# Performance work log

Measured on AMD Instinct MI355X. Metric: run time of the kernel, lower is better.

## Reference

```python
import jax, jax.numpy as jnp
import numpy as np
from jax.scipy.special import logsumexp

L = 15      # DATA_MAX_SEG_LEN
K = 64      # XCRIBE_DIM
H = 16      # SEG_DIM
TAG = 32    # TAG_DIM
DUR = 4     # DURATION_DIM
NY = 15     # len(LABELS)
N = 16384   # sequence length
S = 2048    # number of gold segments
NEG = jnp.float32(-1e30)


def setup_inputs() -> dict:
    key = jax.random.key(0)
    ks = jax.random.split(key, 24)
    sL = 1.0 / np.sqrt(H)
    sV = 1.0 / np.sqrt(2 * H + TAG + DUR)
    sW = 1.0 / np.sqrt(H)

    def U(k, shape, s):
        return jax.random.uniform(k, shape, jnp.float32, -s, s)

    return dict(
        data=jax.random.normal(ks[0], (N, K), jnp.float32),
        fwd_Wih=U(ks[1], (4 * H, K), sL), fwd_Whh=U(ks[2], (4 * H, H), sL),
        fwd_bih=U(ks[3], (4 * H,), sL), fwd_bhh=U(ks[4], (4 * H,), sL),
        bwd_Wih=U(ks[5], (4 * H, K), sL), bwd_Whh=U(ks[6], (4 * H, H), sL),
        bwd_bih=U(ks[7], (4 * H,), sL), bwd_bhh=U(ks[8], (4 * H,), sL),
        fwd_h0=jax.random.normal(ks[9], (H,), jnp.float32),
        fwd_c0=jax.random.normal(ks[10], (H,), jnp.float32),
        bwd_h0=jax.random.normal(ks[11], (H,), jnp.float32),
        bwd_c0=jax.random.normal(ks[12], (H,), jnp.float32),
        Y_enc=jax.random.normal(ks[13], (NY, TAG), jnp.float32),
        Z_enc=jax.random.normal(ks[14], (L, DUR), jnp.float32),
        V_W=U(ks[15], (H, 2 * H + TAG + DUR), sV), V_b=U(ks[16], (H,), sV),
        W_W=U(ks[17], (1, H), sW), W_b=U(ks[18], (1,), sW),
        tags=jax.random.randint(ks[19], (S,), 0, NY),
        lengths=jax.random.randint(ks[20], (S,), 1, L + 1),
    )


def _lstm(xs, Wih, Whh, bih, bhh, h0, c0):
    # xs: [L, B, K] -> hidden outputs [L, B, H]; torch gate order i,f,g,o
    B = xs.shape[1]
    b = bih + bhh

    def step(carry, x):
        h, c = carry
        g = x @ Wih.T + h @ Whh.T + b
        i, f, gg, o = jnp.split(g, 4, axis=-1)
        c = jax.nn.sigmoid(f) * c + jax.nn.sigmoid(i) * jnp.tanh(gg)
        h = jax.nn.sigmoid(o) * jnp.tanh(c)
        return (h, c), h

    init = (jnp.broadcast_to(h0, (B, H)), jnp.broadcast_to(c0, (B, H)))
    _, hs = jax.lax.scan(step, init, xs)
    return hs


def reference(data, fwd_Wih, fwd_Whh, fwd_bih, fwd_bhh, fwd_h0, fwd_c0,
              bwd_Wih, bwd_Whh, bwd_bih, bwd_bhh, bwd_h0, bwd_c0,
              Y_enc, Z_enc, V_W, V_b, W_W, W_b, tags, lengths):
    n = data.shape[0]
    pos = jnp.arange(n)[:, None]      # [N,1]
    dd = jnp.arange(L)[None, :]       # [1,L]
    idx_f = jnp.minimum(pos + dd, n - 1)   # forward window indices
    idx_b = pos - dd                       # backward window indices (may be <0)

    win_f = data[idx_f].transpose(1, 0, 2)                  # [L,N,K]
    win_b = data[jnp.maximum(idx_b, 0)].transpose(1, 0, 2)  # [L,N,K]

    # fwd[i,d] = forward_precalc[i][i+d]; bwd[e,d] = backward_precalc[e-d][e]
    fwd = _lstm(win_f, fwd_Wih, fwd_Whh, fwd_bih, fwd_bhh, fwd_h0, fwd_c0).transpose(1, 0, 2)
    bwd = _lstm(win_b, bwd_Wih, bwd_Whh, bwd_bih, bwd_bhh, bwd_h0, bwd_c0).transpose(1, 0, 2)

    # gather fwd at (start=e-d, duration index d) -> aligned with end position e
    fwd_g = fwd[jnp.maximum(idx_b, 0), dd]          # [N,L,H]
    fb = jnp.concatenate([fwd_g, bwd], axis=-1)     # [N,L,2H]

    # split V across concat blocks: [fwd,bwd | Y | Z]
    V1 = V_W[:, :2 * H]; V2 = V_W[:, 2 * H:2 * H + TAG]; V3 = V_W[:, 2 * H + TAG:]
    base = fb @ V1.T + (Z_enc @ V3.T)[None, :, :] + V_b      # [N,L,H]
    ypart = Y_enc @ V2.T                                     # [NY,H]
    pre = base[:, :, None, :] + ypart[None, None, :, :]      # [N,L,NY,H]
    scores = jnp.tanh(pre) @ W_W[0] + W_b[0]                 # [N,L,NY]

    valid = idx_b >= 0
    A = jnp.where(valid, logsumexp(scores, axis=-1), NEG)    # [N,L] lse over labels

    # semi-Markov forward DP: log_alpha[i] = lse_d(log_alpha[i-d] + A[i-1,d-1])
    def dp(hist, a):  # hist[k] = log_alpha[i-1-k]
        new = logsumexp(hist + a)
        return jnp.concatenate([new[None], hist[:-1]]), new

    hist0 = jnp.full((L,), NEG, jnp.float32).at[0].set(0.0)
    _, alphas = jax.lax.scan(dp, hist0, A)
    logZ = alphas[-1]

    # gold-segment score; original never advances `chars`, so start is always 0
    gv = lengths < L
    gscores = scores[lengths - 1, lengths - 1, tags]
    indiv = jnp.sum(jnp.where(gv, gscores, 0.0))
    return logZ - indiv
```

## Files before the change

kernel.cpp:

```cpp
#include <hip/hip_runtime.h>

#define NPOS 16384
#define NEG  (-1e30f)

#define OFF_FWDH  0
#define OFF_BWDH  1966080
#define OFF_A     3932160
#define OFF_T0    4194304
#define OFF_R     4251904
#define OFF_GSC   4255504
#define OFF_CTR   4255744

struct Params {
    const float *data, *fWih, *fWhh, *fbih, *fbhh, *bWih, *bWhh, *bbih, *bbhh;
    const float *h0f, *c0f, *h0b, *c0b, *Yenc, *Zenc, *VW, *Vb, *WW, *Wb;
    const int *tags, *lengths;
    float *ws; float *out;
};

typedef _Float16 half2_t __attribute__((ext_vector_type(2)));

__device__ __forceinline__ half2_t u2h(unsigned int v) {
    return __builtin_bit_cast(half2_t, v);
}
__device__ __forceinline__ unsigned int packh(float a, float b) {
    half2_t h = { (_Float16)a, (_Float16)b };
    return __builtin_bit_cast(unsigned int, h);
}
__device__ __forceinline__ float fdot2_(unsigned int w, unsigned int x, float acc) {
    return __builtin_amdgcn_fdot2(u2h(w), u2h(x), acc, false);
}
__device__ __forceinline__ float sigf(float x) {
    return __builtin_amdgcn_rcpf(1.0f + __expf(-x));
}
__device__ __forceinline__ float tanhf_(float x) {
    return 1.0f - 2.0f * __builtin_amdgcn_rcpf(1.0f + __expf(2.0f * x));
}
__device__ __forceinline__ float lse15(const float* tv) {
    float a0 = fmaxf(tv[0], tv[1]),  a1 = fmaxf(tv[2], tv[3]);
    float a2 = fmaxf(tv[4], tv[5]),  a3 = fmaxf(tv[6], tv[7]);
    float a4 = fmaxf(tv[8], tv[9]),  a5 = fmaxf(tv[10], tv[11]);
    float a6 = fmaxf(tv[12], tv[13]);
    float b0 = fmaxf(a0, a1), b1 = fmaxf(a2, a3), b2 = fmaxf(a4, a5), b3 = fmaxf(a6, tv[14]);
    float mx = fmaxf(fmaxf(b0, b1), fmaxf(b2, b3));
    float e[15];
    #pragma unroll
    for (int i = 0; i < 15; i++) e[i] = __expf(tv[i] - mx);
    float s0 = e[0]+e[1], s1 = e[2]+e[3], s2 = e[4]+e[5], s3 = e[6]+e[7];
    float s4 = e[8]+e[9], s5 = e[10]+e[11], s6 = e[12]+e[13];
    float t0 = s0+s1, t1 = s2+s3, t2 = s4+s5, t3 = s6+e[14];
    return mx + __logf((t0+t1) + (t2+t3));
}

__global__ __launch_bounds__(512) void kA(Params p)
{
    __shared__ unsigned int xs2[78*33];
    __shared__ float xgT[64*78];
    __shared__ unsigned int hsh[2*512];
    __shared__ unsigned int wqx[2048];
    __shared__ unsigned int wqh[512];
    __shared__ float bq[64];

    const int tid  = threadIdx.x;
    const int lane = tid & 63;
    const int wq   = __builtin_amdgcn_readfirstlane(tid >> 6);
    const int dir  = blockIdx.y;
    const int P0   = blockIdx.x << 6;
    const int dbase = P0 - (dir ? 14 : 0);

    if (blockIdx.x == 0 && dir == 0 && tid == 0)
        ((unsigned int*)(p.ws + OFF_CTR))[0] = 0;

    const float* Wih = dir ? p.bWih : p.fWih;
    const float* Whh = dir ? p.bWhh : p.fWhh;
    const float* bih = dir ? p.bbih : p.fbih;
    const float* bhh = dir ? p.bbhh : p.fbhh;
    const float* h0  = dir ? p.h0b  : p.h0f;
    const float* c0  = dir ? p.c0b  : p.c0f;

    for (int e = tid; e < 2048; e += 512) {
        int k2 = e >> 6, pi = e & 63;
        int w = pi >> 3, jj = pi & 7;
        int j = ((jj >> 1) << 4) + 2*w + (jj & 1);
        wqx[e] = packh(Wih[j*64 + 2*k2], Wih[j*64 + 2*k2 + 1]);
    }
    if (tid < 512) {
        int m2 = tid >> 6, pi = tid & 63;
        int w = pi >> 3, jj = pi & 7;
        int j = ((jj >> 1) << 4) + 2*w + (jj & 1);
        wqh[tid] = packh(Whh[j*16 + 2*m2], Whh[j*16 + 2*m2 + 1]);
    }
    if (tid < 64) {
        int w = tid >> 3, jj = tid & 7;
        int j = ((jj >> 1) << 4) + 2*w + (jj & 1);
        bq[tid] = bih[j] + bhh[j];
    }
    for (int idx = tid; idx < 78*32; idx += 512) {
        int r = idx >> 5, c = idx & 31;
        int q = dbase + r;
        q = q < 0 ? 0 : (q > NPOS-1 ? NPOS-1 : q);
        float2 x2 = *(const float2*)(p.data + (size_t)q*64 + c*2);
        xs2[r*33 + c] = packh(x2.x, x2.y);
    }
    if (tid < 512) {
        int m2 = tid >> 6;
        hsh[tid] = packh(h0[2*m2], h0[2*m2 + 1]);
    }
    __syncthreads();

    #pragma unroll
    for (int pass = 0; pass < 2; pass++) {
        int r = pass*64 + lane;
        if (r < 78) {
            float acc[8];
            #pragma unroll
            for (int jj = 0; jj < 8; jj++) acc[jj] = bq[wq*8 + jj];
            #pragma unroll 8
            for (int k2 = 0; k2 < 32; k2++) {
                unsigned int xp = xs2[r*33 + k2];
                uint4 w0 = *(const uint4*)&wqx[k2*64 + wq*8];
                uint4 w1 = *(const uint4*)&wqx[k2*64 + wq*8 + 4];
                acc[0] = fdot2_(w0.x, xp, acc[0]);
                acc[1] = fdot2_(w0.y, xp, acc[1]);
                acc[2] = fdot2_(w0.z, xp, acc[2]);
                acc[3] = fdot2_(w0.w, xp, acc[3]);
                acc[4] = fdot2_(w1.x, xp, acc[4]);
                acc[5] = fdot2_(w1.y, xp, acc[5]);
                acc[6] = fdot2_(w1.z, xp, acc[6]);
                acc[7] = fdot2_(w1.w, xp, acc[7]);
            }
            #pragma unroll
            for (int jj = 0; jj < 8; jj++) xgT[(wq*8 + jj)*78 + r] = acc[jj];
        }
    }
    float cv0 = c0[wq*2], cv1 = c0[wq*2 + 1];
    unsigned int* outH = (unsigned int*)(p.ws + (dir ? OFF_BWDH : OFF_FWDH));
    __syncthreads();

    int buf = 0;
    for (int d = 0; d < 15; d++) {
        const int row = dir ? (lane + 14 - d) : (lane + d);
        float part[8];
        #pragma unroll
        for (int jj = 0; jj < 8; jj++) part[jj] = xgT[(wq*8 + jj)*78 + row];
        #pragma unroll
        for (int m2 = 0; m2 < 8; m2++) {
            unsigned int hp = hsh[buf*512 + m2*64 + lane];
            uint4 w0 = *(const uint4*)&wqh[m2*64 + wq*8];
            uint4 w1 = *(const uint4*)&wqh[m2*64 + wq*8 + 4];
            part[0] = fdot2_(w0.x, hp, part[0]);
            part[1] = fdot2_(w0.y, hp, part[1]);
            part[2] = fdot2_(w0.z, hp, part[2]);
            part[3] = fdot2_(w0.w, hp, part[3]);
            part[4] = fdot2_(w1.x, hp, part[4]);
            part[5] = fdot2_(w1.y, hp, part[5]);
            part[6] = fdot2_(w1.z, hp, part[6]);
            part[7] = fdot2_(w1.w, hp, part[7]);
        }
        float cn0 = sigf(part[2])*cv0 + sigf(part[0])*tanhf_(part[4]);
        float cn1 = sigf(part[3])*cv1 + sigf(part[1])*tanhf_(part[5]);
        cv0 = cn0; cv1 = cn1;
        float h0v = sigf(part[6])*tanhf_(cn0);
        float h1v = sigf(part[7])*tanhf_(cn1);
        unsigned int pk = packh(h0v, h1v);
        hsh[(buf^1)*512 + wq*64 + lane] = pk;
        outH[((size_t)d*NPOS + P0 + lane)*8 + wq] = pk;
        __syncthreads();
        buf ^= 1;
    }
}

__global__ __launch_bounds__(1024) void kBC(Params p)
{
    __shared__ float As[64*17];
    __shared__ unsigned int VWh[256];
    __shared__ float zbl[240];
    __shared__ float EY[240];
    const int tid = threadIdx.x;
    const int P0  = blockIdx.x << 6;
    float* ws = p.ws;

    if (tid < 240) {
        int y = tid >> 4, h = tid & 15;
        float acc = 0.f;
        for (int t = 0; t < 32; t++) acc += p.Yenc[y*32 + t] * p.VW[h*68 + 32 + t];
        EY[tid] = __expf(acc + acc);
        float z = p.Vb[h];
        for (int u = 0; u < 4; u++) z += p.Zenc[y*4 + u] * p.VW[h*68 + 64 + u];
        zbl[tid] = z;
    }
    if (tid < 256) {
        int h = tid >> 4, j2 = tid & 15;
        int col = (j2 < 8) ? 2*j2 : 16 + 2*(j2 - 8);
        VWh[tid] = packh(p.VW[h*68 + col], p.VW[h*68 + col + 1]);
    }
    __syncthreads();

    const int pl = tid & 63;
    const int d  = tid >> 6;
    const int pp = P0 + pl;
    float Aval = NEG;
    if (d < 15 && pp >= d) {
        const uint4* fptr = (const uint4*)((const unsigned int*)(ws + OFF_FWDH)
                            + ((size_t)d*NPOS + (pp - d))*8);
        const uint4* bptr = (const uint4*)((const unsigned int*)(ws + OFF_BWDH)
                            + ((size_t)d*NPOS + pp)*8);
        uint4 f0 = fptr[0], f1 = fptr[1];
        uint4 b0 = bptr[0], b1 = bptr[1];
        unsigned int fp_[8] = {f0.x, f0.y, f0.z, f0.w, f1.x, f1.y, f1.z, f1.w};
        unsigned int bp_[8] = {b0.x, b0.y, b0.z, b0.w, b1.x, b1.y, b1.z, b1.w};
        float E[16], w2[16], wsum = 0.f;
        #pragma unroll
        for (int h = 0; h < 16; h++) {
            float acc = zbl[d*16 + h];
            uint4 va = *(const uint4*)&VWh[h*16];
            uint4 vb = *(const uint4*)&VWh[h*16 + 4];
            uint4 vc = *(const uint4*)&VWh[h*16 + 8];
            uint4 vd = *(const uint4*)&VWh[h*16 + 12];
            acc = fdot2_(va.x, fp_[0], acc); acc = fdot2_(va.y, fp_[1], acc);
            acc = fdot2_(va.z, fp_[2], acc); acc = fdot2_(va.w, fp_[3], acc);
            acc = fdot2_(vb.x, fp_[4], acc); acc = fdot2_(vb.y, fp_[5], acc);
            acc = fdot2_(vb.z, fp_[6], acc); acc = fdot2_(vb.w, fp_[7], acc);
            acc = fdot2_(vc.x, bp_[0], acc); acc = fdot2_(vc.y, bp_[1], acc);
            acc = fdot2_(vc.z, bp_[2], acc); acc = fdot2_(vc.w, bp_[3], acc);
            acc = fdot2_(vd.x, bp_[4], acc); acc = fdot2_(vd.y, bp_[5], acc);
            acc = fdot2_(vd.z, bp_[6], acc); acc = fdot2_(vd.w, bp_[7], acc);
            E[h] = __expf(acc + acc);
            float w = p.WW[h];
            w2[h] = -2.0f * w;
            wsum += w;
        }
        const float cst = p.Wb[0] + wsum;
        float sc[15];
        #pragma unroll
        for (int y = 0; y < 15; y++) {
            float a = 0.f;
            #pragma unroll
            for (int h = 0; h < 16; h++)
                a = fmaf(w2[h], __builtin_amdgcn_rcpf(1.0f + E[h]*EY[y*16 + h]), a);
            sc[y] = cst + a;
        }
        Aval = lse15(sc);
        if (pp == d && pp < 15) {
            float* gsc = ws + OFF_GSC;
            #pragma unroll
            for (int y = 0; y < 15; y++) gsc[pp*15 + y] = sc[y];
        }
    }
    As[pl*17 + d] = Aval;
    __syncthreads();

    if (tid < 15) {
        const int j = tid;
        float s[15];
        #pragma unroll
        for (int i = 0; i < 15; i++) s[i] = (i == j) ? 0.f : NEG;
        #pragma unroll 4
        for (int t = 0; t < 64; t++) {
            float tv[15];
            #pragma unroll
            for (int i = 0; i < 15; i++) tv[i] = s[i] + As[t*17 + i];
            float nw = lse15(tv);
            #pragma unroll
            for (int i = 14; i > 0; i--) s[i] = s[i-1];
            s[0] = nw;
        }
        float* T0 = ws + OFF_T0;
        #pragma unroll
        for (int i = 0; i < 15; i++) T0[blockIdx.x*225 + i*15 + j] = s[i];
    }
}

__global__ __launch_bounds__(256) void kDE(Params p)
{
    __shared__ float sm[4084];
    __shared__ int lastFlag;
    const int tid = threadIdx.x;
    const int b   = blockIdx.x;
    unsigned int* ctr = (unsigned int*)(p.ws + OFF_CTR);

    {
        float* Rm = sm;
        const float* T0 = p.ws + OFF_T0;
        const int e = tid, i2 = e / 15, j2 = e % 15;
        const int c0 = b * 16;
        if (e < 225) Rm[i2*16 + j2] = T0[c0*225 + e];
        __syncthreads();
        for (int t = 1; t < 16; t++) {
            float nw = 0.f;
            if (e < 225) {
                const float* Trow = T0 + (c0 + t)*225 + i2*15;
                float tv[15];
                #pragma unroll
                for (int k = 0; k < 15; k++) tv[k] = Trow[k] + Rm[k*16 + j2];
                nw = lse15(tv);
            }
            __syncthreads();
            if (e < 225) Rm[i2*16 + j2] = nw;
            __syncthreads();
        }
        if (e < 225) p.ws[OFF_R + b*225 + e] = Rm[i2*16 + j2];
    }
    __syncthreads();
    __threadfence();
    if (tid == 0) {
        unsigned int old = __hip_atomic_fetch_add(&ctr[0], 1u, __ATOMIC_ACQ_REL,
                                                  __HIP_MEMORY_SCOPE_AGENT);
        lastFlag = (old == 15u);
    }
    __syncthreads();
    if (!lastFlag) return;
    __threadfence();

    {
        float* RA  = sm;
        float* G   = sm + 3840;
        float* red = sm + 4080;
        const float* Rg = p.ws + OFF_R;
        for (int idx = tid; idx < 16*225; idx += 256) {
            int t = idx / 225, r = idx % 225;
            RA[t*240 + (r/15)*16 + (r%15)] = Rg[idx];
        }
        __syncthreads();
        const int e = tid, i2 = e / 15, j2 = e % 15;
        if (e < 225) G[i2*16 + j2] = RA[i2*16 + j2];
        __syncthreads();
        for (int t = 1; t < 16; t++) {
            float nw = 0.f;
            if (e < 225) {
                float tv[15];
                #pragma unroll
                for (int k = 0; k < 15; k++) tv[k] = RA[t*240 + i2*16 + k] + G[k*16 + j2];
                nw = lse15(tv);
            }
            __syncthreads();
            if (e < 225) G[i2*16 + j2] = nw;
            __syncthreads();
        }
        const float* gsc = p.ws + OFF_GSC;
        float loc = 0.f;
        for (int s = tid; s < 2048; s += 256) {
            int len = p.lengths[s];
            if (len < 15) loc += gsc[(len-1)*15 + p.tags[s]];
        }
        #pragma unroll
        for (int off = 32; off > 0; off >>= 1) loc += __shfl_down(loc, off);
        if ((tid & 63) == 0) red[tid >> 6] = loc;
        __syncthreads();
        if (tid == 0) {
            float ind = red[0] + red[1] + red[2] + red[3];
            p.out[0] = G[0] - ind;
        }
    }
}

extern "C" void kernel_launch(void* const* d_in, const int* in_sizes, int n_in,
                              void* d_out, int out_size, void* d_ws, size_t ws_size,
                              hipStream_t stream)
{
    Params prm;
    prm.data = (const float*)d_in[0];
    prm.fWih = (const float*)d_in[1];
    prm.fWhh = (const float*)d_in[2];
    prm.fbih = (const float*)d_in[3];
    prm.fbhh = (const float*)d_in[4];
    prm.bWih = (const float*)d_in[5];
    prm.bWhh = (const float*)d_in[6];
    prm.bbih = (const float*)d_in[7];
    prm.bbhh = (const float*)d_in[8];
    prm.h0f  = (const float*)d_in[9];
    prm.c0f  = (const float*)d_in[10];
    prm.h0b  = (const float*)d_in[11];
    prm.c0b  = (const float*)d_in[12];
    prm.Yenc = (const float*)d_in[13];
    prm.Zenc = (const float*)d_in[14];
    prm.VW   = (const float*)d_in[15];
    prm.Vb   = (const float*)d_in[16];
    prm.WW   = (const float*)d_in[17];
    prm.Wb   = (const float*)d_in[18];
    prm.tags    = (const int*)d_in[19];
    prm.lengths = (const int*)d_in[20];
    prm.ws  = (float*)d_ws;
    prm.out = (float*)d_out;

    hipLaunchKernelGGL(kA,  dim3(256, 2), dim3(512),  0, stream, prm);
    hipLaunchKernelGGL(kBC, dim3(256),    dim3(1024), 0, stream, prm);
    hipLaunchKernelGGL(kDE, dim3(16),     dim3(256),  0, stream, prm);
}
```

Before: 187.4 us.

## Fuse chunk-combine into kBC via last-block tree reduction of transfer matrices

Removes the separate kDE launch. The block that finishes last in kBC (found with an atomic counter) now combines all 256 per-chunk 15x15 log-semiring transfer matrices. It does this as a binary tree reduction that ping-pongs between two global workspace buffers. This replaces the earlier two-stage sequential combination (16 blocks of 16 steps, then 16 more serial steps) and saves one kernel launch. In exchange, the whole reduction runs on a single block and goes through global memory, which adds latency between tree levels.

```diff
diff --git a/kernel.cpp b/kernel.cpp
--- a/kernel.cpp
+++ b/kernel.cpp
@@ -10,6 +10,7 @@
 #define OFF_R     4251904
 #define OFF_GSC   4255504
 #define OFF_CTR   4255744
+#define OFF_T1    4260096
 
 struct Params {
     const float *data, *fWih, *fWhh, *fbih, *fbhh, *bWih, *bWhh, *bbih, *bbhh;
@@ -170,12 +171,14 @@
     }
 }
 
-__global__ __launch_bounds__(1024) void kBC(Params p)
+__global__ __launch_bounds__(1024) void kBCD(Params p)
 {
     __shared__ float As[64*17];
     __shared__ unsigned int VWh[256];
     __shared__ float zbl[240];
     __shared__ float EY[240];
+    __shared__ float red[16];
+    __shared__ int lastFlag;
     const int tid = threadIdx.x;
     const int P0  = blockIdx.x << 6;
     float* ws = p.ws;
@@ -269,88 +272,53 @@
         #pragma unroll
         for (int i = 0; i < 15; i++) T0[blockIdx.x*225 + i*15 + j] = s[i];
     }
-}
-
-__global__ __launch_bounds__(256) void kDE(Params p)
-{
-    __shared__ float sm[4084];
-    __shared__ int lastFlag;
-    const int tid = threadIdx.x;
-    const int b   = blockIdx.x;
-    unsigned int* ctr = (unsigned int*)(p.ws + OFF_CTR);
-
-    {
-        float* Rm = sm;
-        const float* T0 = p.ws + OFF_T0;
-        const int e = tid, i2 = e / 15, j2 = e % 15;
-        const int c0 = b * 16;
-        if (e < 225) Rm[i2*16 + j2] = T0[c0*225 + e];
-        __syncthreads();
-        for (int t = 1; t < 16; t++) {
-            float nw = 0.f;
-            if (e < 225) {
-                const float* Trow = T0 + (c0 + t)*225 + i2*15;
-                float tv[15];
-                #pragma unroll
-                for (int k = 0; k < 15; k++) tv[k] = Trow[k] + Rm[k*16 + j2];
-                nw = lse15(tv);
-            }
-            __syncthreads();
-            if (e < 225) Rm[i2*16 + j2] = nw;
-            __syncthreads();
-        }
-        if (e < 225) p.ws[OFF_R + b*225 + e] = Rm[i2*16 + j2];
-    }
     __syncthreads();
     __threadfence();
+    unsigned int* ctr = (unsigned int*)(ws + OFF_CTR);
     if (tid == 0) {
         unsigned int old = __hip_atomic_fetch_add(&ctr[0], 1u, __ATOMIC_ACQ_REL,
                                                   __HIP_MEMORY_SCOPE_AGENT);
-        lastFlag = (old == 15u);
+        lastFlag = (old == 255u);
     }
     __syncthreads();
     if (!lastFlag) return;
     __threadfence();
 
-    {
-        float* RA  = sm;
-        float* G   = sm + 3840;
-        float* red = sm + 4080;
-        const float* Rg = p.ws + OFF_R;
-        for (int idx = tid; idx < 16*225; idx += 256) {
-            int t = idx / 225, r = idx % 225;
-            RA[t*240 + (r/15)*16 + (r%15)] = Rg[idx];
+    float* bufA = ws + OFF_T0;
+    float* bufB = ws + OFF_T1;
+    const float* src = bufA;
+    float* dst = bufB;
+    for (int n = 256; n > 1; n >>= 1) {
+        int half = n >> 1;
+        for (int e = tid; e < half*225; e += 1024) {
+            int cpair = e / 225, r = e % 225;
+            int i2 = r / 15, j2 = r % 15;
+            const float* lo = src + (2*cpair)*225;
+            const float* hi = src + (2*cpair + 1)*225;
+            float tv[15];
+            #pragma unroll
+            for (int k = 0; k < 15; k++) tv[k] = hi[i2*15 + k] + lo[k*15 + j2];
+            dst[e] = lse15(tv);
         }
         __syncthreads();
-        const int e = tid, i2 = e / 15, j2 = e % 15;
-        if (e < 225) G[i2*16 + j2] = RA[i2*16 + j2];
-        __syncthreads();
-        for (int t = 1; t < 16; t++) {
-            float nw = 0.f;
-            if (e < 225) {
-                float tv[15];
-                #pragma unroll
-                for (int k = 0; k < 15; k++) tv[k] = RA[t*240 + i2*16 + k] + G[k*16 + j2];
-                nw = lse15(tv);
-            }
-            __syncthreads();
-            if (e < 225) G[i2*16 + j2] = nw;
-            __syncthreads();
-        }
-        const float* gsc = p.ws + OFF_GSC;
-        float loc = 0.f;
-        for (int s = tid; s < 2048; s += 256) {
-            int len = p.lengths[s];
-            if (len < 15) loc += gsc[(len-1)*15 + p.tags[s]];
-        }
-        #pragma unroll
-        for (int off = 32; off > 0; off >>= 1) loc += __shfl_down(loc, off);
-        if ((tid & 63) == 0) red[tid >> 6] = loc;
-        __syncthreads();
-        if (tid == 0) {
-            float ind = red[0] + red[1] + red[2] + red[3];
-            p.out[0] = G[0] - ind;
-        }
+        const float* ts = dst; dst = (dst == bufB) ? bufA : bufB;
+        src = ts;
+    }
+    const float* gsc = ws + OFF_GSC;
+    float loc = 0.f;
+    for (int s = tid; s < 2048; s += 1024) {
+        int len = p.lengths[s];
+        if (len < 15) loc += gsc[(len-1)*15 + p.tags[s]];
+    }
+    #pragma unroll
+    for (int off = 32; off > 0; off >>= 1) loc += __shfl_down(loc, off);
+    if ((tid & 63) == 0) red[tid >> 6] = loc;
+    __syncthreads();
+    if (tid == 0) {
+        float ind = 0.f;
+        #pragma unroll
+        for (int w = 0; w < 16; w++) ind += red[w];
+        p.out[0] = src[0] - ind;
     }
 }
 
@@ -383,7 +351,6 @@
     prm.ws  = (float*)d_ws;
     prm.out = (float*)d_out;
 
-    hipLaunchKernelGGL(kA,  dim3(256, 2), dim3(512),  0, stream, prm);
-    hipLaunchKernelGGL(kBC, dim3(256),    dim3(1024), 0, stream, prm);
-    hipLaunchKernelGGL(kDE, dim3(16),     dim3(256),  0, stream, prm);
-}
+    hipLaunchKernelGGL(kA,   dim3(256, 2), dim3(512),  0, stream, prm);
+    hipLaunchKernelGGL(kBCD, dim3(256),    dim3(1024), 0, stream, prm);
+}
```

New measurement: 340.7 us. +81.8%, slower.
